# Optimization experiments

Measured on AMD Instinct MI355X. Metric: run time of the kernel, lower is better.

The kernel has to match this reference:

```python
import jax, jax.numpy as jnp
import numpy as np

FRAME = 1024
ENC = 256
HID = 128
EPS = 1e-7


def _lstm_cell(x, h, c, Wih, Whh, bih, bhh):
    # PyTorch LSTM gate order: i, f, g, o
    z = Wih @ x + bih + Whh @ h + bhh  # [4H]
    i, f, g, o = jnp.split(z, 4)
    i = jax.nn.sigmoid(i)
    f = jax.nn.sigmoid(f)
    g = jnp.tanh(g)
    o = jax.nn.sigmoid(o)
    c_new = f * c + i * g
    h_new = o * jnp.tanh(c_new)
    return h_new, c_new


def setup_inputs() -> dict:
    key = jax.random.key(0)
    ks = jax.random.split(key, 20)
    s = 0.05
    return {
        "y1": jax.random.normal(ks[0], (FRAME,), jnp.float32),
        "h1_in": jax.random.normal(ks[1], (HID,), jnp.float32),
        "c1_in": jax.random.normal(ks[2], (HID,), jnp.float32),
        "h2_in": jax.random.normal(ks[3], (HID,), jnp.float32),
        "c2_in": jax.random.normal(ks[4], (HID,), jnp.float32),
        "enc_W": jax.random.normal(ks[5], (ENC, FRAME), jnp.float32) * s,
        "gamma": jnp.ones((ENC,), jnp.float32),
        "beta": jnp.zeros((ENC,), jnp.float32),
        "Wih1": jax.random.normal(ks[6], (4 * HID, ENC), jnp.float32) * s,
        "Whh1": jax.random.normal(ks[7], (4 * HID, HID), jnp.float32) * s,
        "bih1": jax.random.normal(ks[8], (4 * HID,), jnp.float32) * s,
        "bhh1": jax.random.normal(ks[9], (4 * HID,), jnp.float32) * s,
        "Wih2": jax.random.normal(ks[10], (4 * HID, HID), jnp.float32) * s,
        "Whh2": jax.random.normal(ks[11], (4 * HID, HID), jnp.float32) * s,
        "bih2": jax.random.normal(ks[12], (4 * HID,), jnp.float32) * s,
        "bhh2": jax.random.normal(ks[13], (4 * HID,), jnp.float32) * s,
        "dense_W": jax.random.normal(ks[14], (ENC, HID), jnp.float32) * s,
        "dense_b": jax.random.normal(ks[15], (ENC,), jnp.float32) * s,
        "dec_W": jax.random.normal(ks[16], (FRAME, ENC), jnp.float32) * s,
    }


def reference(y1, h1_in, c1_in, h2_in, c2_in, enc_W, gamma, beta,
              Wih1, Whh1, bih1, bhh1, Wih2, Whh2, bih2, bhh2,
              dense_W, dense_b, dec_W):
    # encoder 1x1 conv == matvec: [256,1024] @ [1024]
    enc = enc_W @ y1  # [256]
    # global-statistic instant layer norm (mean/var over ALL elements)
    mean = jnp.mean(enc)
    sub = enc - mean
    var = jnp.mean(jnp.square(sub))
    enc_norm = (sub / jnp.sqrt(var + EPS)) * gamma + beta
    # two stateful LSTM cells (seq_len=1; dropout is identity at inference)
    h1, c1 = _lstm_cell(enc_norm, h1_in, c1_in, Wih1, Whh1, bih1, bhh1)
    h2, c2 = _lstm_cell(h1, h2_in, c2_in, Wih2, Whh2, bih2, bhh2)
    # dense + sigmoid mask on UN-normalized encoded features
    mask = jax.nn.sigmoid(dense_W @ h2 + dense_b)  # [256]
    estimated = mask * enc
    # decoder 1x1 conv == matvec: [1024,256] @ [256]
    decoded = dec_W @ estimated  # [1024]
    return (decoded.reshape(1, FRAME, 1),
            h1.reshape(1, 1, HID), c1.reshape(1, 1, HID),
            h2.reshape(1, 1, HID), c2.reshape(1, 1, HID))
```

## Files before the change

kernel.cpp:

```cpp
#include <hip/hip_runtime.h>
#include <hip/hip_bf16.h>
#include <math.h>


#define FRAME 1024
#define ENC 256
#define HID 128

__device__ __forceinline__ float wave_reduce(float v) {
#pragma unroll
    for (int o = 32; o > 0; o >>= 1) v += __shfl_down(v, o);
    return v;
}

__device__ __forceinline__ float sigmoidf(float x) { return 1.0f / (1.0f + expf(-x)); }

__global__ __launch_bounds__(256) void k_enc(const float* __restrict__ W,
                                             const float* __restrict__ y,
                                             float* __restrict__ enc) {
    const int row = blockIdx.x;
    const int t = threadIdx.x;
    const int lane = t & 63, wid = t >> 6;
    const float4 a = reinterpret_cast<const float4*>(W + row * FRAME)[t];
    const float4 b = reinterpret_cast<const float4*>(y)[t];
    float p = a.x * b.x + a.y * b.y + a.z * b.z + a.w * b.w;
    p = wave_reduce(p);
    __shared__ float red[4];
    if (lane == 0) red[wid] = p;
    __syncthreads();
    if (t == 0) enc[row] = red[0] + red[1] + red[2] + red[3];
}

__global__ __launch_bounds__(256) void k_ln_lstm1(const float* __restrict__ enc,
                                                  const float* __restrict__ gamma,
                                                  const float* __restrict__ beta,
                                                  const float* __restrict__ Wih1,
                                                  const float* __restrict__ Whh1,
                                                  const float* __restrict__ bih1,
                                                  const float* __restrict__ bhh1,
                                                  const float* __restrict__ h1_in,
                                                  float* __restrict__ z1) {
    __shared__ __align__(16) float encn[ENC];
    __shared__ __align__(16) float hsh[HID];
    __shared__ float red[8];
    const int t = threadIdx.x;
    const int lane = t & 63, wid = t >> 6;

    const float e = enc[t];
    float s = wave_reduce(e);
    float s2 = wave_reduce(e * e);
    if (lane == 0) { red[wid] = s; red[4 + wid] = s2; }
    if (t < HID) hsh[t] = h1_in[t];
    __syncthreads();
    const float sum = red[0] + red[1] + red[2] + red[3];
    const float sumsq = red[4] + red[5] + red[6] + red[7];
    const float mean = sum * (1.0f / ENC);
    const float var = sumsq * (1.0f / ENC) - mean * mean;
    const float inv = rsqrtf(var + 1e-7f);
    encn[t] = (e - mean) * inv * gamma[t] + beta[t];
    __syncthreads();

    const int row = blockIdx.x * 4 + wid;
    const float4 a = reinterpret_cast<const float4*>(Wih1 + row * ENC)[lane];
    const float4 b = reinterpret_cast<const float4*>(encn)[lane];
    float p = a.x * b.x + a.y * b.y + a.z * b.z + a.w * b.w;
    const float2 c = reinterpret_cast<const float2*>(Whh1 + row * HID)[lane];
    const float2 d = reinterpret_cast<const float2*>(hsh)[lane];
    p += c.x * d.x + c.y * d.y;
    p = wave_reduce(p);
    if (lane == 0) z1[row] = p + bih1[row] + bhh1[row];
}

__global__ __launch_bounds__(256) void k_lstm2(const float* __restrict__ z1,
                                               const float* __restrict__ c1_in,
                                               const float* __restrict__ h2_in,
                                               const float* __restrict__ Wih2,
                                               const float* __restrict__ Whh2,
                                               const float* __restrict__ bih2,
                                               const float* __restrict__ bhh2,
                                               float* __restrict__ z2,
                                               float* __restrict__ out_h1,
                                               float* __restrict__ out_c1) {
    __shared__ __align__(16) float h1s[HID];
    __shared__ __align__(16) float h2s[HID];
    const int t = threadIdx.x;
    const int lane = t & 63, wid = t >> 6;
    if (t < HID) {
        const float i = sigmoidf(z1[t]);
        const float f = sigmoidf(z1[HID + t]);
        const float g = tanhf(z1[2 * HID + t]);
        const float o = sigmoidf(z1[3 * HID + t]);
        const float c = f * c1_in[t] + i * g;
        const float h = o * tanhf(c);
        h1s[t] = h;
        h2s[t] = h2_in[t];
        if (blockIdx.x == 0) { out_h1[t] = h; out_c1[t] = c; }
    }
    __syncthreads();

    const int row = blockIdx.x * 4 + wid;
    const float2 a = reinterpret_cast<const float2*>(Wih2 + row * HID)[lane];
    const float2 b = reinterpret_cast<const float2*>(h1s)[lane];
    const float2 c = reinterpret_cast<const float2*>(Whh2 + row * HID)[lane];
    const float2 d = reinterpret_cast<const float2*>(h2s)[lane];
    float p = a.x * b.x + a.y * b.y + c.x * d.x + c.y * d.y;
    p = wave_reduce(p);
    if (lane == 0) z2[row] = p + bih2[row] + bhh2[row];
}

__global__ __launch_bounds__(256) void k_mask(const float* __restrict__ z2,
                                              const float* __restrict__ c2_in,
                                              const float* __restrict__ dense_W,
                                              const float* __restrict__ dense_b,
                                              const float* __restrict__ enc,
                                              float* __restrict__ est,
                                              float* __restrict__ out_h2,
                                              float* __restrict__ out_c2) {
    __shared__ __align__(16) float h2sh[HID];
    const int t = threadIdx.x;
    const int lane = t & 63, wid = t >> 6;
    if (t < HID) {
        const float i = sigmoidf(z2[t]);
        const float f = sigmoidf(z2[HID + t]);
        const float g = tanhf(z2[2 * HID + t]);
        const float o = sigmoidf(z2[3 * HID + t]);
        const float c = f * c2_in[t] + i * g;
        const float h = o * tanhf(c);
        h2sh[t] = h;
        if (blockIdx.x == 0) { out_h2[t] = h; out_c2[t] = c; }
    }
    __syncthreads();

    const int row = blockIdx.x * 4 + wid;
    const float2 a = reinterpret_cast<const float2*>(dense_W + row * HID)[lane];
    const float2 b = reinterpret_cast<const float2*>(h2sh)[lane];
    float p = a.x * b.x + a.y * b.y;
    p = wave_reduce(p);
    if (lane == 0) {
        const float m = sigmoidf(p + dense_b[row]);
        est[row] = m * enc[row];
    }
}

__global__ __launch_bounds__(256) void k_dec(const float* __restrict__ dec_W,
                                             const float* __restrict__ est,
                                             float* __restrict__ out) {
    __shared__ __align__(16) float es[ENC];
    const int t = threadIdx.x;
    const int lane = t & 63, wid = t >> 6;
    es[t] = est[t];
    __syncthreads();
    const int row = blockIdx.x * 4 + wid;
    const float4 a = reinterpret_cast<const float4*>(dec_W + row * ENC)[lane];
    const float4 b = reinterpret_cast<const float4*>(es)[lane];
    float p = a.x * b.x + a.y * b.y + a.z * b.z + a.w * b.w;
    p = wave_reduce(p);
    if (lane == 0) out[row] = p;
}

extern "C" void kernel_launch(void* const* d_in, const int* in_sizes, int n_in,
                              void* d_out, int out_size, void* d_ws, size_t ws_size,
                              hipStream_t stream) {
    const float* y1      = (const float*)d_in[0];
    const float* h1_in   = (const float*)d_in[1];
    const float* c1_in   = (const float*)d_in[2];
    const float* h2_in   = (const float*)d_in[3];
    const float* c2_in   = (const float*)d_in[4];
    const float* enc_W   = (const float*)d_in[5];
    const float* gamma   = (const float*)d_in[6];
    const float* beta    = (const float*)d_in[7];
    const float* Wih1    = (const float*)d_in[8];
    const float* Whh1    = (const float*)d_in[9];
    const float* bih1    = (const float*)d_in[10];
    const float* bhh1    = (const float*)d_in[11];
    const float* Wih2    = (const float*)d_in[12];
    const float* Whh2    = (const float*)d_in[13];
    const float* bih2    = (const float*)d_in[14];
    const float* bhh2    = (const float*)d_in[15];
    const float* dense_W = (const float*)d_in[16];
    const float* dense_b = (const float*)d_in[17];
    const float* dec_W   = (const float*)d_in[18];

    float* out = (float*)d_out;
    float* ws  = (float*)d_ws;
    float* enc = ws;
    float* z1  = ws + 256;
    float* z2  = ws + 768;
    float* est = ws + 1280;

    k_enc<<<256, 256, 0, stream>>>(enc_W, y1, enc);
    k_ln_lstm1<<<128, 256, 0, stream>>>(enc, gamma, beta, Wih1, Whh1, bih1, bhh1, h1_in, z1);
    k_lstm2<<<128, 256, 0, stream>>>(z1, c1_in, h2_in, Wih2, Whh2, bih2, bhh2, z2,
                                     out + FRAME, out + FRAME + HID);
    k_mask<<<64, 256, 0, stream>>>(z2, c2_in, dense_W, dense_b, enc, est,
                                   out + FRAME + 2 * HID, out + FRAME + 3 * HID);
    k_dec<<<256, 256, 0, stream>>>(dec_W, est, out);
}
```

Baseline: 19.63 us.

## Fuse five matvec kernels into one cooperative kernel with grid syncs

Replaces the five separate kernel launches with a single cooperative kernel of 64 blocks that uses grid-wide syncs between the encoder, LSTM1, LSTM2 and mask/decoder stages. Each block handles more rows per stage, and every block redundantly computes the full dense+mask vector into shared memory, which removes one stage boundary. The aim is to cut launch and inter-kernel gaps, at the cost of grid.sync overhead and less parallelism for the bandwidth-bound matvecs.

```diff
diff --git a/kernel.cpp b/kernel.cpp
--- a/kernel.cpp
+++ b/kernel.cpp
@@ -1,11 +1,14 @@
 #include <hip/hip_runtime.h>
-#include <hip/hip_bf16.h>
+#include <hip/hip_cooperative_groups.h>
 #include <math.h>
+
+namespace cg = cooperative_groups;
 
 
 #define FRAME 1024
 #define ENC 256
 #define HID 128
+#define NBLK 64
 
 __device__ __forceinline__ float wave_reduce(float v) {
 #pragma unroll
@@ -15,147 +18,137 @@
 
 __device__ __forceinline__ float sigmoidf(float x) { return 1.0f / (1.0f + expf(-x)); }
 
-__global__ __launch_bounds__(256) void k_enc(const float* __restrict__ W,
-                                             const float* __restrict__ y,
-                                             float* __restrict__ enc) {
-    const int row = blockIdx.x;
-    const int t = threadIdx.x;
-    const int lane = t & 63, wid = t >> 6;
-    const float4 a = reinterpret_cast<const float4*>(W + row * FRAME)[t];
-    const float4 b = reinterpret_cast<const float4*>(y)[t];
-    float p = a.x * b.x + a.y * b.y + a.z * b.z + a.w * b.w;
-    p = wave_reduce(p);
-    __shared__ float red[4];
-    if (lane == 0) red[wid] = p;
-    __syncthreads();
-    if (t == 0) enc[row] = red[0] + red[1] + red[2] + red[3];
-}
+__global__ __launch_bounds__(256) void k_fused(
+    const float* __restrict__ y1, const float* __restrict__ h1_in,
+    const float* __restrict__ c1_in, const float* __restrict__ h2_in,
+    const float* __restrict__ c2_in, const float* __restrict__ enc_W,
+    const float* __restrict__ gamma, const float* __restrict__ beta,
+    const float* __restrict__ Wih1, const float* __restrict__ Whh1,
+    const float* __restrict__ bih1, const float* __restrict__ bhh1,
+    const float* __restrict__ Wih2, const float* __restrict__ Whh2,
+    const float* __restrict__ bih2, const float* __restrict__ bhh2,
+    const float* __restrict__ dense_W, const float* __restrict__ dense_b,
+    const float* __restrict__ dec_W, float* __restrict__ out,
+    float* __restrict__ ws)
+{
+    cg::grid_group grid = cg::this_grid();
+    const int t = threadIdx.x, lane = t & 63, wid = t >> 6, bid = blockIdx.x;
+    float* enc_g = ws;
+    float* z1    = ws + 256;
+    float* z2    = ws + 768;
 
-__global__ __launch_bounds__(256) void k_ln_lstm1(const float* __restrict__ enc,
-                                                  const float* __restrict__ gamma,
-                                                  const float* __restrict__ beta,
-                                                  const float* __restrict__ Wih1,
-                                                  const float* __restrict__ Whh1,
-                                                  const float* __restrict__ bih1,
-                                                  const float* __restrict__ bhh1,
-                                                  const float* __restrict__ h1_in,
-                                                  float* __restrict__ z1) {
     __shared__ __align__(16) float encn[ENC];
-    __shared__ __align__(16) float hsh[HID];
+    __shared__ __align__(16) float hA[HID];
+    __shared__ __align__(16) float hB[HID];
+    __shared__ __align__(16) float es[ENC];
     __shared__ float red[8];
-    const int t = threadIdx.x;
-    const int lane = t & 63, wid = t >> 6;
 
-    const float e = enc[t];
-    float s = wave_reduce(e);
-    float s2 = wave_reduce(e * e);
-    if (lane == 0) { red[wid] = s; red[4 + wid] = s2; }
-    if (t < HID) hsh[t] = h1_in[t];
-    __syncthreads();
-    const float sum = red[0] + red[1] + red[2] + red[3];
-    const float sumsq = red[4] + red[5] + red[6] + red[7];
-    const float mean = sum * (1.0f / ENC);
-    const float var = sumsq * (1.0f / ENC) - mean * mean;
-    const float inv = rsqrtf(var + 1e-7f);
-    encn[t] = (e - mean) * inv * gamma[t] + beta[t];
-    __syncthreads();
+    {
+        const int row = bid * 4 + wid;
+        const float4* Wr = reinterpret_cast<const float4*>(enc_W + row * FRAME);
+        const float4* Y  = reinterpret_cast<const float4*>(y1);
+        float p = 0.f;
+#pragma unroll
+        for (int k = 0; k < 4; ++k) {
+            const float4 a = Wr[k * 64 + lane];
+            const float4 b = Y[k * 64 + lane];
+            p += a.x * b.x + a.y * b.y + a.z * b.z + a.w * b.w;
+        }
+        p = wave_reduce(p);
+        if (lane == 0) enc_g[row] = p;
+    }
+    grid.sync();
 
-    const int row = blockIdx.x * 4 + wid;
-    const float4 a = reinterpret_cast<const float4*>(Wih1 + row * ENC)[lane];
-    const float4 b = reinterpret_cast<const float4*>(encn)[lane];
-    float p = a.x * b.x + a.y * b.y + a.z * b.z + a.w * b.w;
-    const float2 c = reinterpret_cast<const float2*>(Whh1 + row * HID)[lane];
-    const float2 d = reinterpret_cast<const float2*>(hsh)[lane];
-    p += c.x * d.x + c.y * d.y;
-    p = wave_reduce(p);
-    if (lane == 0) z1[row] = p + bih1[row] + bhh1[row];
-}
+    {
+        const float e = enc_g[t];
+        const float s  = wave_reduce(e);
+        const float s2 = wave_reduce(e * e);
+        if (lane == 0) { red[wid] = s; red[4 + wid] = s2; }
+        if (t < HID) hA[t] = h1_in[t];
+        __syncthreads();
+        const float mean = (red[0] + red[1] + red[2] + red[3]) * (1.f / ENC);
+        const float var  = (red[4] + red[5] + red[6] + red[7]) * (1.f / ENC) - mean * mean;
+        const float inv  = rsqrtf(var + 1e-7f);
+        encn[t] = (e - mean) * inv * gamma[t] + beta[t];
+        __syncthreads();
+#pragma unroll
+        for (int j = 0; j < 2; ++j) {
+            const int row = bid * 8 + wid * 2 + j;
+            const float4 a = reinterpret_cast<const float4*>(Wih1 + row * ENC)[lane];
+            const float4 b = reinterpret_cast<const float4*>(encn)[lane];
+            float p = a.x * b.x + a.y * b.y + a.z * b.z + a.w * b.w;
+            const float2 c = reinterpret_cast<const float2*>(Whh1 + row * HID)[lane];
+            const float2 d = reinterpret_cast<const float2*>(hA)[lane];
+            p += c.x * d.x + c.y * d.y;
+            p = wave_reduce(p);
+            if (lane == 0) z1[row] = p + bih1[row] + bhh1[row];
+        }
+    }
+    grid.sync();
 
-__global__ __launch_bounds__(256) void k_lstm2(const float* __restrict__ z1,
-                                               const float* __restrict__ c1_in,
-                                               const float* __restrict__ h2_in,
-                                               const float* __restrict__ Wih2,
-                                               const float* __restrict__ Whh2,
-                                               const float* __restrict__ bih2,
-                                               const float* __restrict__ bhh2,
-                                               float* __restrict__ z2,
-                                               float* __restrict__ out_h1,
-                                               float* __restrict__ out_c1) {
-    __shared__ __align__(16) float h1s[HID];
-    __shared__ __align__(16) float h2s[HID];
-    const int t = threadIdx.x;
-    const int lane = t & 63, wid = t >> 6;
-    if (t < HID) {
-        const float i = sigmoidf(z1[t]);
-        const float f = sigmoidf(z1[HID + t]);
-        const float g = tanhf(z1[2 * HID + t]);
-        const float o = sigmoidf(z1[3 * HID + t]);
-        const float c = f * c1_in[t] + i * g;
-        const float h = o * tanhf(c);
-        h1s[t] = h;
-        h2s[t] = h2_in[t];
-        if (blockIdx.x == 0) { out_h1[t] = h; out_c1[t] = c; }
+    {
+        if (t < HID) {
+            const float i = sigmoidf(z1[t]);
+            const float f = sigmoidf(z1[HID + t]);
+            const float g = tanhf(z1[2 * HID + t]);
+            const float o = sigmoidf(z1[3 * HID + t]);
+            const float c = f * c1_in[t] + i * g;
+            const float h = o * tanhf(c);
+            hA[t] = h;
+            hB[t] = h2_in[t];
+            if (bid == 0) { out[FRAME + t] = h; out[FRAME + HID + t] = c; }
+        }
+        __syncthreads();
+#pragma unroll
+        for (int j = 0; j < 2; ++j) {
+            const int row = bid * 8 + wid * 2 + j;
+            const float2 a = reinterpret_cast<const float2*>(Wih2 + row * HID)[lane];
+            const float2 b = reinterpret_cast<const float2*>(hA)[lane];
+            const float2 c = reinterpret_cast<const float2*>(Whh2 + row * HID)[lane];
+            const float2 d = reinterpret_cast<const float2*>(hB)[lane];
+            float p = a.x * b.x + a.y * b.y + c.x * d.x + c.y * d.y;
+            p = wave_reduce(p);
+            if (lane == 0) z2[row] = p + bih2[row] + bhh2[row];
+        }
     }
-    __syncthreads();
+    grid.sync();
 
-    const int row = blockIdx.x * 4 + wid;
-    const float2 a = reinterpret_cast<const float2*>(Wih2 + row * HID)[lane];
-    const float2 b = reinterpret_cast<const float2*>(h1s)[lane];
-    const float2 c = reinterpret_cast<const float2*>(Whh2 + row * HID)[lane];
-    const float2 d = reinterpret_cast<const float2*>(h2s)[lane];
-    float p = a.x * b.x + a.y * b.y + c.x * d.x + c.y * d.y;
-    p = wave_reduce(p);
-    if (lane == 0) z2[row] = p + bih2[row] + bhh2[row];
-}
-
-__global__ __launch_bounds__(256) void k_mask(const float* __restrict__ z2,
-                                              const float* __restrict__ c2_in,
-                                              const float* __restrict__ dense_W,
-                                              const float* __restrict__ dense_b,
-                                              const float* __restrict__ enc,
-                                              float* __restrict__ est,
-                                              float* __restrict__ out_h2,
-                                              float* __restrict__ out_c2) {
-    __shared__ __align__(16) float h2sh[HID];
-    const int t = threadIdx.x;
-    const int lane = t & 63, wid = t >> 6;
-    if (t < HID) {
-        const float i = sigmoidf(z2[t]);
-        const float f = sigmoidf(z2[HID + t]);
-        const float g = tanhf(z2[2 * HID + t]);
-        const float o = sigmoidf(z2[3 * HID + t]);
-        const float c = f * c2_in[t] + i * g;
-        const float h = o * tanhf(c);
-        h2sh[t] = h;
-        if (blockIdx.x == 0) { out_h2[t] = h; out_c2[t] = c; }
+    {
+        if (t < HID) {
+            const float i = sigmoidf(z2[t]);
+            const float f = sigmoidf(z2[HID + t]);
+            const float g = tanhf(z2[2 * HID + t]);
+            const float o = sigmoidf(z2[3 * HID + t]);
+            const float c = f * c2_in[t] + i * g;
+            const float h = o * tanhf(c);
+            hB[t] = h;
+            if (bid == 0) { out[FRAME + 2 * HID + t] = h; out[FRAME + 3 * HID + t] = c; }
+        }
+        __syncthreads();
+        {
+            const float4* wr = reinterpret_cast<const float4*>(dense_W + t * HID);
+            const float4* hv = reinterpret_cast<const float4*>(hB);
+            float p = 0.f;
+#pragma unroll
+            for (int k = 0; k < HID / 4; ++k) {
+                const float4 a = wr[k];
+                const float4 b = hv[k];
+                p += a.x * b.x + a.y * b.y + a.z * b.z + a.w * b.w;
+            }
+            const float m = sigmoidf(p + dense_b[t]);
+            es[t] = m * enc_g[t];
+        }
+        __syncthreads();
+#pragma unroll
+        for (int j = 0; j < 4; ++j) {
+            const int row = bid * 16 + wid * 4 + j;
+            const float4 a = reinterpret_cast<const float4*>(dec_W + row * ENC)[lane];
+            const float4 b = reinterpret_cast<const float4*>(es)[lane];
+            float p = a.x * b.x + a.y * b.y + a.z * b.z + a.w * b.w;
+            p = wave_reduce(p);
+            if (lane == 0) out[row] = p;
+        }
     }
-    __syncthreads();
-
-    const int row = blockIdx.x * 4 + wid;
-    const float2 a = reinterpret_cast<const float2*>(dense_W + row * HID)[lane];
-    const float2 b = reinterpret_cast<const float2*>(h2sh)[lane];
-    float p = a.x * b.x + a.y * b.y;
-    p = wave_reduce(p);
-    if (lane == 0) {
-        const float m = sigmoidf(p + dense_b[row]);
-        est[row] = m * enc[row];
-    }
-}
-
-__global__ __launch_bounds__(256) void k_dec(const float* __restrict__ dec_W,
-                                             const float* __restrict__ est,
-                                             float* __restrict__ out) {
-    __shared__ __align__(16) float es[ENC];
-    const int t = threadIdx.x;
-    const int lane = t & 63, wid = t >> 6;
-    es[t] = est[t];
-    __syncthreads();
-    const int row = blockIdx.x * 4 + wid;
-    const float4 a = reinterpret_cast<const float4*>(dec_W + row * ENC)[lane];
-    const float4 b = reinterpret_cast<const float4*>(es)[lane];
-    float p = a.x * b.x + a.y * b.y + a.z * b.z + a.w * b.w;
-    p = wave_reduce(p);
-    if (lane == 0) out[row] = p;
 }
 
 extern "C" void kernel_launch(void* const* d_in, const int* in_sizes, int n_in,
@@ -183,16 +176,14 @@
 
     float* out = (float*)d_out;
     float* ws  = (float*)d_ws;
-    float* enc = ws;
-    float* z1  = ws + 256;
-    float* z2  = ws + 768;
-    float* est = ws + 1280;
 
-    k_enc<<<256, 256, 0, stream>>>(enc_W, y1, enc);
-    k_ln_lstm1<<<128, 256, 0, stream>>>(enc, gamma, beta, Wih1, Whh1, bih1, bhh1, h1_in, z1);
-    k_lstm2<<<128, 256, 0, stream>>>(z1, c1_in, h2_in, Wih2, Whh2, bih2, bhh2, z2,
-                                     out + FRAME, out + FRAME + HID);
-    k_mask<<<64, 256, 0, stream>>>(z2, c2_in, dense_W, dense_b, enc, est,
-                                   out + FRAME + 2 * HID, out + FRAME + 3 * HID);
-    k_dec<<<256, 256, 0, stream>>>(dec_W, est, out);
+    void* args[] = {
+        (void*)&y1, (void*)&h1_in, (void*)&c1_in, (void*)&h2_in, (void*)&c2_in,
+        (void*)&enc_W, (void*)&gamma, (void*)&beta,
+        (void*)&Wih1, (void*)&Whh1, (void*)&bih1, (void*)&bhh1,
+        (void*)&Wih2, (void*)&Whh2, (void*)&bih2, (void*)&bhh2,
+        (void*)&dense_W, (void*)&dense_b, (void*)&dec_W,
+        (void*)&out, (void*)&ws
+    };
+    hipLaunchCooperativeKernel((void*)k_fused, dim3(NBLK), dim3(256), args, 0, stream);
 }
```

Result: slower. 55.43 us (+182.4%).
